# Performance work log

Measured on AMD Instinct MI355X. Metric: run time of the kernel, lower is better.

## Reference

```python
import jax, jax.numpy as jnp
import numpy as np

B, LQ, LK, D, H, DK = 128, 32, 128, 1024, 16, 64


def setup_inputs() -> dict:
    key = jax.random.key(0)
    ks = jax.random.split(key, 10)
    Q_seq = jax.random.normal(ks[0], (B, LQ, D), dtype=jnp.float32)
    K_seq = jax.random.normal(ks[1], (B, LK, D), dtype=jnp.float32)
    V_seq = jax.random.normal(ks[2], (B, LK, D), dtype=jnp.float32)
    title_mask = (jax.random.uniform(ks[3], (B, LQ)) < 0.9).astype(jnp.float32)
    body_mask = (jax.random.uniform(ks[4], (B, LQ, LK)) < 0.9).astype(jnp.float32)
    s = 1.0 / np.sqrt(D)
    Wq = jax.random.uniform(ks[5], (H * DK, D), jnp.float32, -s, s)
    Wk = jax.random.uniform(ks[6], (H * DK, D), jnp.float32, -s, s)
    Wv = jax.random.uniform(ks[7], (H * DK, D), jnp.float32, -s, s)
    bq = jnp.zeros((H * DK,), jnp.float32)
    bk = jnp.zeros((H * DK,), jnp.float32)
    bv = jnp.zeros((H * DK,), jnp.float32)
    return {"Q_seq": Q_seq, "K_seq": K_seq, "V_seq": V_seq,
            "title_mask": title_mask, "body_mask": body_mask,
            "Wq": Wq, "bq": bq, "Wk": Wk, "bk": bk, "Wv": Wv, "bv": bv}


def reference(Q_seq, K_seq, V_seq, title_mask, body_mask, Wq, bq, Wk, bk, Wv, bv):
    b = Q_seq.shape[0]
    # concatenate title tokens onto keys/values: [B, LK+LQ, D]
    K_cat = jnp.concatenate([K_seq, Q_seq], axis=1)
    V_cat = jnp.concatenate([V_seq, Q_seq], axis=1)
    # mask: [B, LQ, LK+LQ]
    tmask_rep = jnp.broadcast_to(title_mask[:, None, :], (b, LQ, LQ))
    mask = jnp.concatenate([body_mask, tmask_rep], axis=2) * title_mask[:, :, None]
    # projections -> [B, H, len, DK]
    Qh = (Q_seq @ Wq.T + bq).reshape(b, LQ, H, DK).transpose(0, 2, 1, 3)
    Kh = (K_cat @ Wk.T + bk).reshape(b, LK + LQ, H, DK).transpose(0, 2, 1, 3)
    Vh = (V_cat @ Wv.T + bv).reshape(b, LK + LQ, H, DK).transpose(0, 2, 1, 3)
    # custom exp-based masked attention (non-softmax normalization)
    scores = jnp.einsum('bhqd,bhkd->bhqk', Qh, Kh) / np.sqrt(float(DK))
    scores = jnp.exp(scores) * mask[:, None, :, :]
    attn = scores / (jnp.sum(scores, axis=-1, keepdims=True) + 1e-8)
    ctx = jnp.einsum('bhqk,bhkd->bhqd', attn, Vh)
    return ctx.transpose(0, 2, 1, 3).reshape(b, LQ, H * DK)
```

## Files before the change

### kernel.cpp

```cpp
#include <hip/hip_runtime.h>

typedef _Float16 f16;
typedef _Float16 f16x4 __attribute__((ext_vector_type(4)));
typedef _Float16 f16x8 __attribute__((ext_vector_type(8)));
typedef float f32x4v __attribute__((ext_vector_type(4)));

#define AS1 __attribute__((address_space(1)))
#define AS3 __attribute__((address_space(3)))

__device__ __forceinline__ void gload_lds16(const f16* g, f16* l) {
  __builtin_amdgcn_global_load_lds((const AS1 unsigned int*)g,
                                   (AS3 unsigned int*)l, 16, 0, 0);
}

__global__ __launch_bounds__(256) void prep_w(
    const float* __restrict__ Wq, const float* __restrict__ Wk,
    const float* __restrict__ Wv,
    f16* __restrict__ Wqb, f16* __restrict__ Wkb, f16* __restrict__ Wvb)
{
  const long long g = (long long)blockIdx.x * 256 + threadIdx.x;
  const float* s;
  f16* d;
  if (g < 131072) {
    s = Wq + g * 8; d = Wqb + g * 8;
  } else if (g < 262144) {
    long long e = (g - 131072) * 8; s = Wk + e; d = Wkb + e;
  } else {
    long long e = (g - 262144) * 8; s = Wv + e; d = Wvb + e;
  }
  float4 v0 = *(const float4*)s;
  float4 v1 = *(const float4*)(s + 4);
  f16x8 o;
  o[0] = (f16)v0.x; o[1] = (f16)v0.y; o[2] = (f16)v0.z; o[3] = (f16)v0.w;
  o[4] = (f16)v1.x; o[5] = (f16)v1.y; o[6] = (f16)v1.z; o[7] = (f16)v1.w;
  *(f16x8*)d = o;
}

__device__ __forceinline__ void gemm_tile_128_f32A(
    const float* __restrict__ A, const f16* __restrict__ W,
    const float* __restrict__ bias, f16* __restrict__ C,
    int m0, int n0, int rowShift, int outStride, int rowOff,
    f16* sbuf)
{
  const int t = threadIdx.x;
  const int w = t >> 6, lane = t & 63;
  const int wr = w >> 1, wc = w & 1;
  const int fr = lane & 15, g = lane >> 4;

  const int arow4 = lane >> 4;
  const int ax = w * 4 + arow4;
  const float* aSrc = A + (long long)(m0 + ax) * 1024 + ((lane & 15) ^ ax) * 4;

  const int brow = lane >> 3;
  const f16* bSrc = W + (long long)(n0 + w * 8 + brow) * 1024 +
                    ((lane & 7) ^ brow) * 8;

  const float* Asl = (const float*)sbuf;
  const f16* Bsl = sbuf + 16384;

  const int aoff = (wr * 64 + fr) * 64;
  const int boff = (wc * 64 + fr) * 64;
  const int gkB0 = ((0 + g) ^ (fr & 7)) * 8;
  const int gkB1 = ((4 + g) ^ (fr & 7)) * 8;
  const int pa0 = ((2 * g) ^ fr) * 4;
  const int pa1 = ((2 * (4 + g)) ^ fr) * 4;
  const bool pa_sw = (fr & 1);

  f32x4v acc[4][4];
#pragma unroll
  for (int i = 0; i < 4; ++i)
#pragma unroll
    for (int j = 0; j < 4; ++j) acc[i][j] = (f32x4v){0.f, 0.f, 0.f, 0.f};

#define CVT8(dst, p)                                                         \
  {                                                                          \
    float4 q0_ = *(const float4*)(p);                                        \
    float4 q1_ = *(const float4*)((p) + ((pa_sw) ? -4 : 4));                 \
    dst[0] = (f16)q0_.x; dst[1] = (f16)q0_.y;                                \
    dst[2] = (f16)q0_.z; dst[3] = (f16)q0_.w;                                \
    dst[4] = (f16)q1_.x; dst[5] = (f16)q1_.y;                                \
    dst[6] = (f16)q1_.z; dst[7] = (f16)q1_.w;                                \
  }

  for (int tt = 0; tt < 16; ++tt) {
    const int ko = tt * 64;
#pragma unroll
    for (int s = 0; s < 8; ++s)
      gload_lds16((const f16*)(aSrc + (long long)s * 16 * 1024 + ko),
                  sbuf + (s * 4 + w) * 512);
#pragma unroll
    for (int s = 0; s < 4; ++s)
      gload_lds16(bSrc + (long long)s * 32 * 1024 + ko,
                  sbuf + 16384 + (s * 4 + w) * 512);
    __syncthreads();

    f16x8 af[4], bf[4];
#pragma unroll
    for (int i = 0; i < 4; ++i) {
      const float* p = Asl + aoff + i * 1024 + pa0;
      CVT8(af[i], p);
    }
#pragma unroll
    for (int j = 0; j < 4; ++j)
      bf[j] = *(const f16x8*)(Bsl + boff + j * 1024 + gkB0);
#pragma unroll
    for (int i = 0; i < 4; ++i)
#pragma unroll
      for (int j = 0; j < 4; ++j)
        acc[i][j] = __builtin_amdgcn_mfma_f32_16x16x32_f16(af[i], bf[j],
                                                           acc[i][j], 0, 0, 0);
#pragma unroll
    for (int i = 0; i < 4; ++i) {
      const float* p = Asl + aoff + i * 1024 + pa1;
      CVT8(af[i], p);
    }
#pragma unroll
    for (int j = 0; j < 4; ++j)
      bf[j] = *(const f16x8*)(Bsl + boff + j * 1024 + gkB1);
#pragma unroll
    for (int i = 0; i < 4; ++i)
#pragma unroll
      for (int j = 0; j < 4; ++j)
        acc[i][j] = __builtin_amdgcn_mfma_f32_16x16x32_f16(af[i], bf[j],
                                                           acc[i][j], 0, 0, 0);

    __syncthreads();
  }
#undef CVT8

  f16* Cs = sbuf;
  float bn[4];
#pragma unroll
  for (int j = 0; j < 4; ++j) bn[j] = bias[n0 + wc * 64 + j * 16 + fr];
#pragma unroll
  for (int i = 0; i < 4; ++i) {
#pragma unroll
    for (int j = 0; j < 4; ++j) {
#pragma unroll
      for (int v = 0; v < 4; ++v) {
        int row = wr * 64 + i * 16 + g * 4 + v;
        int col = wc * 64 + j * 16 + fr;
        Cs[row * 136 + (col ^ ((row & 12) << 2))] = (f16)(acc[i][j][v] + bn[j]);
      }
    }
  }
  __syncthreads();

  const int rowMask = (1 << rowShift) - 1;
  const int row = t >> 1, half = t & 1;
  const int rsw = (row & 12) << 2;
  const int arow = m0 + row;
  const int orow = (arow >> rowShift) * outStride + (arow & rowMask) + rowOff;
  f16* dst = C + (long long)orow * 1024 + n0 + half * 64;
  const f16* srcr = Cs + row * 136;
#pragma unroll
  for (int c = 0; c < 8; ++c)
    *(f16x8*)(dst + c * 8) = *(const f16x8*)(srcr + ((half * 64 + c * 8) ^ rsw));
}

__global__ __launch_bounds__(256) void gemm_all(
    const float* __restrict__ Q_seq, const float* __restrict__ K_seq,
    const float* __restrict__ V_seq,
    const f16* __restrict__ Wqb, const f16* __restrict__ Wkb,
    const f16* __restrict__ Wvb,
    const float* __restrict__ bq, const float* __restrict__ bk,
    const float* __restrict__ bv,
    f16* __restrict__ Qh, f16* __restrict__ Kh, f16* __restrict__ Vh)
{
  __shared__ __align__(16) f16 sbuf[24576];
  const int bid = blockIdx.x;
  const int v = (bid & 7) * 352 + (bid >> 3);

  const float* A;
  const f16* W;
  const float* bias;
  f16* C;
  int m0, n0, rowShift, outStride, rowOff;

  if (v < 2048) {
    const int z = v >> 10, rem = v & 1023;
    A = z ? V_seq : K_seq;
    W = z ? Wvb : Wkb;
    bias = z ? bv : bk;
    C = z ? Vh : Kh;
    m0 = (rem >> 3) * 128; n0 = (rem & 7) * 128;
    rowShift = 7; outStride = 160; rowOff = 0;
  } else {
    const int u = v - 2048;
    const int z = u >> 8, rem = u & 255;
    A = Q_seq;
    W = (z == 0) ? Wqb : (z == 1) ? Wkb : Wvb;
    bias = (z == 0) ? bq : (z == 1) ? bk : bv;
    C = (z == 0) ? Qh : (z == 1) ? Kh : Vh;
    m0 = (rem >> 3) * 128; n0 = (rem & 7) * 128;
    rowShift = 5;
    outStride = (z == 0) ? 32 : 160;
    rowOff = (z == 0) ? 0 : 128;
  }
  gemm_tile_128_f32A(A, W, bias, C, m0, n0, rowShift, outStride, rowOff, sbuf);
}

__global__ __launch_bounds__(256) void attn_kernel(
    const f16* __restrict__ Qh, const f16* __restrict__ Kh,
    const f16* __restrict__ Vh,
    const float* __restrict__ title, const float* __restrict__ body,
    float* __restrict__ out)
{
  __shared__ __align__(16) f16 Qs[32 * 72];
  __shared__ __align__(16) f16 Ks[160 * 72];
  __shared__ __align__(16) f16 Vs[160 * 68];
  __shared__ float rs[4][32];
  __shared__ float invs[32];

  const int bh = blockIdx.x, b = bh >> 4, h = bh & 15;
  const int t = threadIdx.x, w = t >> 6, lane = t & 63;
  const int c = lane & 15, g = lane >> 4;

  const long long qbase = ((long long)(b * 32) << 10) + h * 64;
  const long long kbase = ((long long)(b * 160) << 10) + h * 64;

  {
    int row = t >> 3, ch = t & 7;
    *(f16x8*)(Qs + row * 72 + ch * 8) =
        *(const f16x8*)(Qh + qbase + (long long)row * 1024 + ch * 8);
  }
#pragma unroll
  for (int r = 0; r < 5; ++r) {
    int i = t + r * 256;
    int row = i >> 3, ch = i & 7;
    *(f16x8*)(Ks + row * 72 + ch * 8) =
        *(const f16x8*)(Kh + kbase + (long long)row * 1024 + ch * 8);
    f16x8 vv = *(const f16x8*)(Vh + kbase + (long long)row * 1024 + ch * 8);
    f16x4 vlo = __builtin_shufflevector(vv, vv, 0, 1, 2, 3);
    f16x4 vhi = __builtin_shufflevector(vv, vv, 4, 5, 6, 7);
    *(f16x4*)(Vs + row * 68 + ch * 8) = vlo;
    *(f16x4*)(Vs + row * 68 + ch * 8 + 4) = vhi;
  }
  __syncthreads();

  f16x8 qf[2][2];
#pragma unroll
  for (int qt = 0; qt < 2; ++qt)
#pragma unroll
    for (int s = 0; s < 2; ++s)
      qf[qt][s] = *(const f16x8*)(Qs + (qt * 16 + c) * 72 + s * 32 + g * 8);

  const int cnt = (w < 2) ? 3 : 2;
  const int tile0 = (w < 2) ? w * 3 : 6 + (w - 2) * 2;

  f16x4 pp[3][2];
  float rsum[2] = {0.f, 0.f};

#pragma unroll
  for (int i = 0; i < 3; ++i) {
    if (i < cnt) {
      const int kt = tile0 + i;
      f16x8 kf0 = *(const f16x8*)(Ks + (kt * 16 + c) * 72 + 0 + g * 8);
      f16x8 kf1 = *(const f16x8*)(Ks + (kt * 16 + c) * 72 + 32 + g * 8);
#pragma unroll
      for (int qt = 0; qt < 2; ++qt) {
        f32x4v s4 = (f32x4v){0.f, 0.f, 0.f, 0.f};
        s4 = __builtin_amdgcn_mfma_f32_16x16x32_f16(kf0, qf[qt][0], s4, 0, 0, 0);
        s4 = __builtin_amdgcn_mfma_f32_16x16x32_f16(kf1, qf[qt][1], s4, 0, 0, 0);
        float4 m4;
        if (kt < 8) {
          m4 = *(const float4*)(body +
                ((long long)(b * 32 + qt * 16 + c)) * 128 + kt * 16 + 4 * g);
        } else {
          m4 = *(const float4*)(title + b * 32 + (kt - 8) * 16 + 4 * g);
        }
        float e0 = __expf(s4[0] * 0.125f) * m4.x;
        float e1 = __expf(s4[1] * 0.125f) * m4.y;
        float e2 = __expf(s4[2] * 0.125f) * m4.z;
        float e3 = __expf(s4[3] * 0.125f) * m4.w;
        rsum[qt] += (e0 + e1) + (e2 + e3);
        f16x4 p4;
        p4.x = (f16)e0; p4.y = (f16)e1; p4.z = (f16)e2; p4.w = (f16)e3;
        pp[i][qt] = p4;
      }
    }
  }

#pragma unroll
  for (int qt = 0; qt < 2; ++qt) {
    rsum[qt] += __shfl_xor(rsum[qt], 16);
    rsum[qt] += __shfl_xor(rsum[qt], 32);
  }
  if (lane < 16) {
    rs[w][c] = rsum[0];
    rs[w][16 + c] = rsum[1];
  }
  __syncthreads();

  f16* Ps = Ks;
#pragma unroll
  for (int i = 0; i < 3; ++i) {
    if (i < cnt) {
      const int kt = tile0 + i;
#pragma unroll
      for (int qt = 0; qt < 2; ++qt)
        *(f16x4*)(Ps + (qt * 16 + c) * 168 + kt * 16 + 4 * g) = pp[i][qt];
    }
  }
  if (t < 32) {
    float ssum = rs[0][t] + rs[1][t] + rs[2][t] + rs[3][t];
    invs[t] = title[b * 32 + t] / (ssum + 1e-8f);
  }
  __syncthreads();

  f32x4v o[2] = {(f32x4v){0.f, 0.f, 0.f, 0.f}, (f32x4v){0.f, 0.f, 0.f, 0.f}};
#pragma unroll
  for (int s = 0; s < 5; ++s) {
    f16x8 vf;
#pragma unroll
    for (int j = 0; j < 8; ++j)
      vf[j] = Vs[(32 * s + 8 * g + j) * 68 + 16 * w + c];
#pragma unroll
    for (int qt = 0; qt < 2; ++qt) {
      f16x8 pf = *(const f16x8*)(Ps + (qt * 16 + c) * 168 + s * 32 + g * 8);
      o[qt] = __builtin_amdgcn_mfma_f32_16x16x32_f16(pf, vf, o[qt], 0, 0, 0);
    }
  }

#pragma unroll
  for (int qt = 0; qt < 2; ++qt) {
#pragma unroll
    for (int v = 0; v < 4; ++v) {
      int q = qt * 16 + 4 * g + v;
      out[((long long)(b * 32 + q) << 10) + h * 64 + 16 * w + c] =
          o[qt][v] * invs[q];
    }
  }
}

extern "C" void kernel_launch(void* const* d_in, const int* in_sizes, int n_in,
                              void* d_out, int out_size, void* d_ws, size_t ws_size,
                              hipStream_t stream) {
  const float* Q_seq = (const float*)d_in[0];
  const float* K_seq = (const float*)d_in[1];
  const float* V_seq = (const float*)d_in[2];
  const float* title = (const float*)d_in[3];
  const float* body  = (const float*)d_in[4];
  const float* Wq = (const float*)d_in[5];
  const float* bq = (const float*)d_in[6];
  const float* Wk = (const float*)d_in[7];
  const float* bk = (const float*)d_in[8];
  const float* Wv = (const float*)d_in[9];
  const float* bv = (const float*)d_in[10];
  float* out = (float*)d_out;

  f16* ws = (f16*)d_ws;
  f16* Wqb = ws;
  f16* Wkb = Wqb + 1048576;
  f16* Wvb = Wkb + 1048576;
  f16* Qh  = Wvb + 1048576;
  f16* Kh  = Qh + 4194304;
  f16* Vh  = Kh + 20971520;

  prep_w<<<1536, 256, 0, stream>>>(Wq, Wk, Wv, Wqb, Wkb, Wvb);
  gemm_all<<<2816, 256, 0, stream>>>(Q_seq, K_seq, V_seq, Wqb, Wkb, Wvb,
                                     bq, bk, bv, Qh, Kh, Vh);
  attn_kernel<<<2048, 256, 0, stream>>>(Qh, Kh, Vh, title, body, out);
}
```

Before: 182.5 us.

## Stage fp32 A tile through registers, converting to fp16 into double-buffered LDS

The A operand (fp32 activations) was previously copied raw into LDS with direct global-to-LDS loads, and each MFMA fragment read converted fp32 to fp16 from LDS. Now each thread loads the next k-tile of A into registers during the current iteration, converts it once to fp16 after the MFMAs, and writes it into a double-buffered fp16 LDS region. This halves LDS traffic and footprint for A, removes redundant conversions, and overlaps the A global load with compute. The cost is 32 extra VGPRs per thread for the prefetch, plus VALU work and LDS writes inside the main loop.

```diff
diff --git a/kernel.cpp b/kernel.cpp
--- a/kernel.cpp
+++ b/kernel.cpp
@@ -36,7 +36,7 @@
   *(f16x8*)d = o;
 }
 
-__device__ __forceinline__ void gemm_tile_128_f32A(
+__device__ __forceinline__ void gemm_tile_128_regA(
     const float* __restrict__ A, const f16* __restrict__ W,
     const float* __restrict__ bias, f16* __restrict__ C,
     int m0, int n0, int rowShift, int outStride, int rowOff,
@@ -47,24 +47,19 @@
   const int wr = w >> 1, wc = w & 1;
   const int fr = lane & 15, g = lane >> 4;
 
-  const int arow4 = lane >> 4;
-  const int ax = w * 4 + arow4;
-  const float* aSrc = A + (long long)(m0 + ax) * 1024 + ((lane & 15) ^ ax) * 4;
+  const int arow = t >> 1, ahalf = t & 1;
+  const float* aSrc = A + (long long)(m0 + arow) * 1024 + ahalf * 32;
+  f16* aDst = sbuf + arow * 64;
 
   const int brow = lane >> 3;
   const f16* bSrc = W + (long long)(n0 + w * 8 + brow) * 1024 +
                     ((lane & 7) ^ brow) * 8;
-
-  const float* Asl = (const float*)sbuf;
   const f16* Bsl = sbuf + 16384;
 
   const int aoff = (wr * 64 + fr) * 64;
   const int boff = (wc * 64 + fr) * 64;
-  const int gkB0 = ((0 + g) ^ (fr & 7)) * 8;
-  const int gkB1 = ((4 + g) ^ (fr & 7)) * 8;
-  const int pa0 = ((2 * g) ^ fr) * 4;
-  const int pa1 = ((2 * (4 + g)) ^ fr) * 4;
-  const bool pa_sw = (fr & 1);
+  const int gk0 = ((0 + g) ^ (fr & 7)) * 8;
+  const int gk1 = ((4 + g) ^ (fr & 7)) * 8;
 
   f32x4v acc[4][4];
 #pragma unroll
@@ -72,37 +67,43 @@
 #pragma unroll
     for (int j = 0; j < 4; ++j) acc[i][j] = (f32x4v){0.f, 0.f, 0.f, 0.f};
 
-#define CVT8(dst, p)                                                         \
+  float4 v[8];
+#define ALOAD(ko_)                                                           \
+  _Pragma("unroll") for (int j = 0; j < 8; ++j)                              \
+      v[j] = *(const float4*)(aSrc + (ko_) + j * 4);
+#define AWRITE(buf_)                                                         \
   {                                                                          \
-    float4 q0_ = *(const float4*)(p);                                        \
-    float4 q1_ = *(const float4*)((p) + ((pa_sw) ? -4 : 4));                 \
-    dst[0] = (f16)q0_.x; dst[1] = (f16)q0_.y;                                \
-    dst[2] = (f16)q0_.z; dst[3] = (f16)q0_.w;                                \
-    dst[4] = (f16)q1_.x; dst[5] = (f16)q1_.y;                                \
-    dst[6] = (f16)q1_.z; dst[7] = (f16)q1_.w;                                \
-  }
+    f16* db_ = aDst + (buf_) * 8192;                                         \
+    _Pragma("unroll") for (int j = 0; j < 4; ++j) {                          \
+      f16x8 hv_;                                                             \
+      hv_[0] = (f16)v[2 * j].x;     hv_[1] = (f16)v[2 * j].y;                \
+      hv_[2] = (f16)v[2 * j].z;     hv_[3] = (f16)v[2 * j].w;                \
+      hv_[4] = (f16)v[2 * j + 1].x; hv_[5] = (f16)v[2 * j + 1].y;            \
+      hv_[6] = (f16)v[2 * j + 1].z; hv_[7] = (f16)v[2 * j + 1].w;            \
+      *(f16x8*)(db_ + (((ahalf * 4 + j) ^ (arow & 7)) * 8)) = hv_;           \
+    }                                                                        \
+  }
+
+  ALOAD(0);
+  AWRITE(0);
 
   for (int tt = 0; tt < 16; ++tt) {
     const int ko = tt * 64;
-#pragma unroll
-    for (int s = 0; s < 8; ++s)
-      gload_lds16((const f16*)(aSrc + (long long)s * 16 * 1024 + ko),
-                  sbuf + (s * 4 + w) * 512);
 #pragma unroll
     for (int s = 0; s < 4; ++s)
       gload_lds16(bSrc + (long long)s * 32 * 1024 + ko,
                   sbuf + 16384 + (s * 4 + w) * 512);
+    if (tt < 15) ALOAD(ko + 64);
     __syncthreads();
 
+    const f16* Ab = sbuf + (tt & 1) * 8192;
     f16x8 af[4], bf[4];
 #pragma unroll
-    for (int i = 0; i < 4; ++i) {
-      const float* p = Asl + aoff + i * 1024 + pa0;
-      CVT8(af[i], p);
-    }
+    for (int i = 0; i < 4; ++i)
+      af[i] = *(const f16x8*)(Ab + aoff + i * 1024 + gk0);
 #pragma unroll
     for (int j = 0; j < 4; ++j)
-      bf[j] = *(const f16x8*)(Bsl + boff + j * 1024 + gkB0);
+      bf[j] = *(const f16x8*)(Bsl + boff + j * 1024 + gk0);
 #pragma unroll
     for (int i = 0; i < 4; ++i)
 #pragma unroll
@@ -110,13 +111,11 @@
         acc[i][j] = __builtin_amdgcn_mfma_f32_16x16x32_f16(af[i], bf[j],
                                                            acc[i][j], 0, 0, 0);
 #pragma unroll
-    for (int i = 0; i < 4; ++i) {
-      const float* p = Asl + aoff + i * 1024 + pa1;
-      CVT8(af[i], p);
-    }
+    for (int i = 0; i < 4; ++i)
+      af[i] = *(const f16x8*)(Ab + aoff + i * 1024 + gk1);
 #pragma unroll
     for (int j = 0; j < 4; ++j)
-      bf[j] = *(const f16x8*)(Bsl + boff + j * 1024 + gkB1);
+      bf[j] = *(const f16x8*)(Bsl + boff + j * 1024 + gk1);
 #pragma unroll
     for (int i = 0; i < 4; ++i)
 #pragma unroll
@@ -124,9 +123,12 @@
         acc[i][j] = __builtin_amdgcn_mfma_f32_16x16x32_f16(af[i], bf[j],
                                                            acc[i][j], 0, 0, 0);
 
+    if (tt < 15) AWRITE((tt + 1) & 1);
+
     __syncthreads();
   }
-#undef CVT8
+#undef ALOAD
+#undef AWRITE
 
   f16* Cs = sbuf;
   float bn[4];
@@ -137,10 +139,11 @@
 #pragma unroll
     for (int j = 0; j < 4; ++j) {
 #pragma unroll
-      for (int v = 0; v < 4; ++v) {
-        int row = wr * 64 + i * 16 + g * 4 + v;
+      for (int v2 = 0; v2 < 4; ++v2) {
+        int row = wr * 64 + i * 16 + g * 4 + v2;
         int col = wc * 64 + j * 16 + fr;
-        Cs[row * 136 + (col ^ ((row & 12) << 2))] = (f16)(acc[i][j][v] + bn[j]);
+        Cs[row * 136 + (col ^ ((row & 12) << 2))] =
+            (f16)(acc[i][j][v2] + bn[j]);
       }
     }
   }
@@ -149,8 +152,8 @@
   const int rowMask = (1 << rowShift) - 1;
   const int row = t >> 1, half = t & 1;
   const int rsw = (row & 12) << 2;
-  const int arow = m0 + row;
-  const int orow = (arow >> rowShift) * outStride + (arow & rowMask) + rowOff;
+  const int crow = m0 + row;
+  const int orow = (crow >> rowShift) * outStride + (crow & rowMask) + rowOff;
   f16* dst = C + (long long)orow * 1024 + n0 + half * 64;
   const f16* srcr = Cs + row * 136;
 #pragma unroll
@@ -197,7 +200,7 @@
     outStride = (z == 0) ? 32 : 160;
     rowOff = (z == 0) ? 0 : 128;
   }
-  gemm_tile_128_f32A(A, W, bias, C, m0, n0, rowShift, outStride, rowOff, sbuf);
+  gemm_tile_128_regA(A, W, bias, C, m0, n0, rowShift, outStride, rowOff, sbuf);
 }
 
 __global__ __launch_bounds__(256) void attn_kernel(
```

Result: slower. 309.4 us (+69.5%).
